# Performance work log

Measured on AMD Instinct MI355X. Metric: run time of the kernel, lower is better.

The kernel has to match this reference:

```python
import jax, jax.numpy as jnp
import numpy as np

N, K = 50000, 64
HID, H = 256, 8
D = HID // H


def setup_inputs() -> dict:
    key = jax.random.key(0)
    ks = jax.random.split(key, 8)
    x = jax.random.normal(ks[0], (N, HID), dtype=jnp.float32)
    neighbor_idx = jax.random.randint(ks[1], (N, K), 0, N, dtype=jnp.int64 if jax.config.jax_enable_x64 else jnp.int32)
    neighbor_mask = jax.random.randint(ks[2], (N, K), 0, 2) == 1  # True = PAD (ignored)
    s = 1.0 / np.sqrt(HID)
    Wq = jax.random.normal(ks[3], (HID, HID), dtype=jnp.float32) * s
    Wk = jax.random.normal(ks[4], (HID, HID), dtype=jnp.float32) * s
    Wv = jax.random.normal(ks[5], (HID, HID), dtype=jnp.float32) * s
    Wo = jax.random.normal(ks[6], (HID, HID), dtype=jnp.float32) * s
    bo = jax.random.normal(ks[7], (HID,), dtype=jnp.float32) * 0.01
    return {"x": x, "neighbor_idx": neighbor_idx, "neighbor_mask": neighbor_mask,
            "Wq": Wq, "Wk": Wk, "Wv": Wv, "Wo": Wo, "bo": bo}


def reference(x, neighbor_idx, neighbor_mask, Wq, Wk, Wv, Wo, bo):
    n, k = neighbor_idx.shape
    scale = jnp.asarray(D, x.dtype) ** -0.5
    # projections (torch nn.Linear: y = x @ W.T)
    q = (x @ Wq.T).reshape(n, H, D)          # [N, H, D]
    k_all = x @ Wk.T                          # [N, HID]
    v_all = x @ Wv.T
    # gather neighbor K/V: [N, k, H, D]
    k_neigh = k_all[neighbor_idx].reshape(n, k, H, D)
    v_neigh = v_all[neighbor_idx].reshape(n, k, H, D)
    # per-node attention scores: [N, H, k]
    scores = jnp.einsum('nhd,nkhd->nhk', q, k_neigh) * scale
    scores = jnp.where(neighbor_mask[:, None, :], -jnp.inf, scores)
    attn = jax.nn.softmax(scores, axis=-1)
    attn = jnp.nan_to_num(attn, nan=0.0)      # rows with all-PAD neighbors -> 0
    out = jnp.einsum('nhk,nkhd->nhd', attn, v_neigh).reshape(n, HID)
    return out @ Wo.T + bo
```

## Files before the change

kernel.cpp:

```cpp
#include <hip/hip_runtime.h>


typedef __bf16 bf16x8 __attribute__((ext_vector_type(8)));
typedef float f32x4 __attribute__((ext_vector_type(4)));
typedef _Float16 h2 __attribute__((ext_vector_type(2)));

#define NN 50000
#define MP 50048
#define MPE ((size_t)MP * 256)
#define QSCALE 0.17677669529663687f

__device__ __forceinline__ float bfl(unsigned u) { return __builtin_bit_cast(float, u << 16); }
__device__ __forceinline__ float bfh(unsigned u) { return __builtin_bit_cast(float, u & 0xFFFF0000u); }
__device__ __forceinline__ unsigned short f2bf(float f) {
    unsigned u = __builtin_bit_cast(unsigned, f);
    return (unsigned short)((u + 0x7FFFu + ((u >> 16) & 1u)) >> 16);
}
__device__ __forceinline__ unsigned pack2(float a, float b) {
    return (unsigned)f2bf(a) | ((unsigned)f2bf(b) << 16);
}
__device__ __forceinline__ void gload16(const void* g, void* l) {
    __builtin_amdgcn_global_load_lds((const __attribute__((address_space(1))) void*)g,
                                     (__attribute__((address_space(3))) void*)l, 16, 0, 0);
}
template <int CTRL>
__device__ __forceinline__ float dpp_add(float x) {
    int yi = __builtin_amdgcn_update_dpp(0, __builtin_bit_cast(int, x), CTRL, 0xF, 0xF, true);
    return x + __builtin_bit_cast(float, yi);
}
template <int CTRL>
__device__ __forceinline__ float dpp_max(float x) {
    int yi = __builtin_amdgcn_update_dpp(0, __builtin_bit_cast(int, x), CTRL, 0xF, 0xF, true);
    return fmaxf(x, __builtin_bit_cast(float, yi));
}
__device__ __forceinline__ float dot2h(unsigned a, unsigned b, float c) {
    return __builtin_amdgcn_fdot2(__builtin_bit_cast(h2, a), __builtin_bit_cast(h2, b), c, false);
}

__global__ __launch_bounds__(256) void prep_k(const float* __restrict__ Wq, const float* __restrict__ Wk,
                                              const float* __restrict__ Wv, const float* __restrict__ Wo,
                                              unsigned short* __restrict__ wqkv, unsigned short* __restrict__ wob,
                                              const void* __restrict__ idxp, const void* __restrict__ maskp,
                                              int* __restrict__ flags) {
    int t = blockIdx.x * 256 + threadIdx.x;
    if (t < 196608) {
        int j = t >> 8, i = t & 255;
        const float* W = (j < 256) ? Wq : (j < 512 ? Wk : Wv);
        wqkv[t] = f2bf(W[((size_t)(j & 255) << 8) | i]);
    } else {
        int u = t - 196608;
        wob[u] = f2bf(Wo[u]);
    }
    if (blockIdx.x == 0) {
        __shared__ int nI32, nF32, nHi;
        if (threadIdx.x == 0) { nI32 = 0; nF32 = 0; nHi = 0; }
        __syncthreads();
        const unsigned* mw = (const unsigned*)maskp;
        const unsigned* iw = (const unsigned*)idxp;
        int a = 0, b = 0, c = 0;
        for (int q = threadIdx.x; q < 1024; q += 256) {
            unsigned v = mw[q];
            if (v > 1u) a = 1;
            if (v != 0u && v != 0x3F800000u) b = 1;
            if (iw[2 * q + 1] != 0u) c = 1;
        }
        if (a) atomicOr(&nI32, 1);
        if (b) atomicOr(&nF32, 1);
        if (c) atomicOr(&nHi, 1);
        __syncthreads();
        if (threadIdx.x == 0) {
            flags[0] = (nI32 == 0) ? 1 : ((nF32 == 0) ? 2 : 0);
            flags[1] = (nHi == 0) ? 1 : 0;
        }
    }
}

__global__ __launch_bounds__(256) void convx_k(const float* __restrict__ x, unsigned short* __restrict__ xb) {
    size_t t = (size_t)blockIdx.x * 256 + threadIdx.x;
    size_t e = t * 8;
    uint4 o;
    if (e < (size_t)NN * 256) {
        float4 a = *(const float4*)&x[e];
        float4 b = *(const float4*)&x[e + 4];
        o.x = pack2(a.x, a.y); o.y = pack2(a.z, a.w);
        o.z = pack2(b.x, b.y); o.w = pack2(b.z, b.w);
    } else {
        o = make_uint4(0, 0, 0, 0);
    }
    *(uint4*)&xb[e] = o;
}

template <int MODE>
__global__ __launch_bounds__(256)
void gemm_bt(const unsigned short* __restrict__ A, const unsigned short* __restrict__ B,
             unsigned short* __restrict__ qkv, float* __restrict__ out, const float* __restrict__ bo) {
    const int tid = threadIdx.x;
    const int wv = tid >> 6, ln = tid & 63;
    const int m0 = blockIdx.x * 128, n0 = blockIdx.y * 128;
    const int wr = wv >> 1, wc = wv & 1;
    __shared__ unsigned short As[2][128][32];
    __shared__ unsigned short Bs[2][128][32];
    f32x4 acc[4][4] = {};

    const int srow = 16 * wv + (ln >> 2);
    #define STAGE(buf, kt)                                                                     \
        {                                                                                      \
            const int col = (kt) * 32 + (ln & 3) * 8;                                          \
            _Pragma("unroll")                                                                  \
            for (int r = 0; r < 2; ++r) {                                                      \
                gload16(&A[(size_t)(m0 + 64 * r + srow) * 256 + col], &As[buf][64 * r + 16 * wv][0]); \
                gload16(&B[(size_t)(n0 + 64 * r + srow) * 256 + col], &Bs[buf][64 * r + 16 * wv][0]); \
            }                                                                                  \
        }

    STAGE(0, 0);
    const int lr = ln & 15, lk = (ln >> 4) * 8;
    for (int kt = 0; kt < 8; ++kt) {
        const int cur = kt & 1;
        __syncthreads();
        if (kt < 7) STAGE(cur ^ 1, kt + 1);
        bf16x8 af[4], bfr[4];
        #pragma unroll
        for (int i = 0; i < 4; ++i) {
            af[i]  = *reinterpret_cast<const bf16x8*>(&As[cur][wr * 64 + i * 16 + lr][lk]);
            bfr[i] = *reinterpret_cast<const bf16x8*>(&Bs[cur][wc * 64 + i * 16 + lr][lk]);
        }
        #pragma unroll
        for (int mi = 0; mi < 4; ++mi)
            #pragma unroll
            for (int ni = 0; ni < 4; ++ni)
                acc[mi][ni] = __builtin_amdgcn_mfma_f32_16x16x32_bf16(af[mi], bfr[ni], acc[mi][ni], 0, 0, 0);
        __syncthreads();
    }

    const int rbase = m0 + wr * 64 + (ln >> 4) * 4;
    const int cbase = n0 + wc * 64 + (ln & 15);
    #pragma unroll
    for (int mi = 0; mi < 4; ++mi) {
        #pragma unroll
        for (int ni = 0; ni < 4; ++ni) {
            const int gn = cbase + ni * 16;
            #pragma unroll
            for (int j = 0; j < 4; ++j) {
                const int gm = rbase + mi * 16 + j;
                float v = acc[mi][ni][j];
                if (MODE == 0) {
                    const float vs = (gn < 256) ? v * QSCALE : v;
                    qkv[(size_t)(gn >> 8) * MPE + (size_t)gm * 256 + (gn & 255)] =
                        __builtin_bit_cast(unsigned short, (_Float16)vs);
                } else {
                    if (gm < NN) out[(size_t)gm * 256 + gn] = v + bo[gn];
                }
            }
        }
    }
    #undef STAGE
}

__global__ __launch_bounds__(256, 3) void attn_k(const unsigned short* __restrict__ qb,
                                                 const unsigned short* __restrict__ kb,
                                                 const unsigned short* __restrict__ vb,
                                                 const void* __restrict__ idxp, const void* __restrict__ maskp,
                                                 unsigned short* __restrict__ attb, const int* __restrict__ flags) {
    const int wv = threadIdx.x >> 6, ln = threadIdx.x & 63;
    const int node = blockIdx.x * 4 + wv;
    const int mlay = flags[0], i64 = flags[1];
    const size_t eb = (size_t)node * 64 + ln;

    int idx = i64 ? ((const int*)idxp)[2 * eb] : ((const int*)idxp)[eb];
    int padi;
    if (mlay == 1)       padi = (((const int*)maskp)[eb] != 0);
    else if (mlay == 2)  padi = (((const unsigned*)maskp)[eb] != 0u);
    else                 padi = (((const unsigned char*)maskp)[eb] != 0);
    const unsigned long long pm = __ballot(padi);
    const int idx_eff = padi ? node : idx;

    const uint2 qv = *(const uint2*)&qb[(size_t)node * 256 + ln * 4];

    const int p = ln & 7;

    uint2 ka[64];
    #pragma unroll
    for (int k = 0; k < 64; ++k) {
        const unsigned nk = (unsigned)__builtin_amdgcn_readlane(idx_eff, k);
        ka[k] = *((const uint2*)(kb + ((size_t)nk << 8)) + ln);
    }
    __builtin_amdgcn_sched_barrier(0);

    float s[8];
    #pragma unroll
    for (int k = 0; k < 64; ++k) {
        const uint2 kv = ka[k];
        float part = dot2h(qv.x, kv.x, dot2h(qv.y, kv.y, 0.0f));
        part = dpp_add<0xB1>(part);
        part = dpp_add<0x4E>(part);
        part = dpp_add<0x141>(part);
        const float sc = ((pm >> k) & 1ull) ? -1e30f : part;
        if ((k & 7) == p) s[k >> 3] = sc;
    }

    uint2 va[64];
    #pragma unroll
    for (int k = 0; k < 64; ++k) {
        const unsigned nk = (unsigned)__builtin_amdgcn_readlane(idx_eff, k);
        va[k] = *((const uint2*)(vb + ((size_t)nk << 8)) + ln);
    }
    __builtin_amdgcn_sched_barrier(0);

    float m = s[0];
    #pragma unroll
    for (int r = 1; r < 8; ++r) m = fmaxf(m, s[r]);
    m = dpp_max<0xB1>(m); m = dpp_max<0x4E>(m); m = dpp_max<0x141>(m);
    float w[8], sum = 0.f;
    #pragma unroll
    for (int r = 0; r < 8; ++r) { w[r] = __expf(s[r] - m); sum += w[r]; }
    sum = dpp_add<0xB1>(sum); sum = dpp_add<0x4E>(sum); sum = dpp_add<0x141>(sum);
    const float inv = (m > -1e29f && sum > 0.f) ? 1.0f / sum : 0.0f;
    #pragma unroll
    for (int r = 0; r < 8; ++r) w[r] *= inv;

    float o0 = 0.f, o1 = 0.f, o2 = 0.f, o3 = 0.f;
    const int baddr = (ln & 56) * 4;
    #pragma unroll
    for (int k = 0; k < 64; ++k) {
        const int wi = __builtin_amdgcn_ds_bpermute(baddr + 4 * (k & 7),
                                                    __builtin_bit_cast(int, w[k >> 3]));
        const float wk = __builtin_bit_cast(float, wi);
        const h2 vx = __builtin_bit_cast(h2, va[k].x);
        const h2 vy = __builtin_bit_cast(h2, va[k].y);
        o0 += wk * (float)vx.x; o1 += wk * (float)vx.y;
        o2 += wk * (float)vy.x; o3 += wk * (float)vy.y;
    }
    uint2 ov;
    ov.x = pack2(o0, o1);
    ov.y = pack2(o2, o3);
    *(uint2*)&attb[(size_t)node * 256 + ln * 4] = ov;
}

extern "C" void kernel_launch(void* const* d_in, const int* in_sizes, int n_in,
                              void* d_out, int out_size, void* d_ws, size_t ws_size,
                              hipStream_t stream) {
    const float* x   = (const float*)d_in[0];
    const void*  idx = d_in[1];
    const void*  msk = d_in[2];
    const float* Wq  = (const float*)d_in[3];
    const float* Wk  = (const float*)d_in[4];
    const float* Wv  = (const float*)d_in[5];
    const float* Wo  = (const float*)d_in[6];
    const float* bo  = (const float*)d_in[7];
    float* out = (float*)d_out;

    unsigned short* xb   = (unsigned short*)d_ws;
    unsigned short* qb   = xb + MPE;
    unsigned short* kb   = qb + MPE;
    unsigned short* vb   = kb + MPE;
    unsigned short* attb = vb + MPE;
    unsigned short* wqkv = attb + MPE;
    unsigned short* wob  = wqkv + 768 * 256;
    int* flags = (int*)(wob + 256 * 256);

    prep_k<<<1024, 256, 0, stream>>>(Wq, Wk, Wv, Wo, wqkv, wob, idx, msk, flags);
    convx_k<<<6256, 256, 0, stream>>>(x, xb);
    gemm_bt<0><<<dim3(391, 6), 256, 0, stream>>>(xb, wqkv, qb, nullptr, nullptr);
    attn_k<<<12500, 256, 0, stream>>>(qb, kb, vb, idx, msk, attb, flags);
    gemm_bt<1><<<dim3(391, 2), 256, 0, stream>>>(attb, wob, nullptr, out, bo);
}
```

Baseline: 430.8 us.

## Restructure QK scoring so each lane computes full per-head dots with pipelined K loads

```diff
diff --git a/kernel.cpp b/kernel.cpp
--- a/kernel.cpp
+++ b/kernel.cpp
@@ -173,31 +173,55 @@
     else if (mlay == 2)  padi = (((const unsigned*)maskp)[eb] != 0u);
     else                 padi = (((const unsigned char*)maskp)[eb] != 0);
     const unsigned long long pm = __ballot(padi);
-    const int idx_eff = padi ? node : idx;
-
-    const uint2 qv = *(const uint2*)&qb[(size_t)node * 256 + ln * 4];
-
-    const int p = ln & 7;
-
-    uint2 ka[64];
-    #pragma unroll
-    for (int k = 0; k < 64; ++k) {
-        const unsigned nk = (unsigned)__builtin_amdgcn_readlane(idx_eff, k);
-        ka[k] = *((const uint2*)(kb + ((size_t)nk << 8)) + ln);
-    }
+    int idx_eff = padi ? node : idx;
+
+    const int h = ln >> 3, j = ln & 7;
+    const int hoff = h << 6;
+    const unsigned mlo = (unsigned)pm, mhi = (unsigned)(pm >> 32);
+
+    const char* qrow = (const char*)qb + (((size_t)node) << 9) + hoff;
+    const uint4 q0 = *(const uint4*)(qrow);
+    const uint4 q1 = *(const uint4*)(qrow + 16);
+    const uint4 q2 = *(const uint4*)(qrow + 32);
+    const uint4 q3 = *(const uint4*)(qrow + 48);
+
+    const char* kbase = (const char*)kb;
+    uint4 kr[3][4];
+    #define KISSUE(buf, c)                                                                \
+        {                                                                                 \
+            const int nk = __builtin_amdgcn_ds_bpermute(4 * j + 32 * (c), idx_eff);       \
+            const unsigned vo = ((unsigned)nk << 9) + hoff;                               \
+            kr[buf][0] = *(const uint4*)(kbase + vo);                                     \
+            kr[buf][1] = *(const uint4*)(kbase + vo + 16);                                \
+            kr[buf][2] = *(const uint4*)(kbase + vo + 32);                                \
+            kr[buf][3] = *(const uint4*)(kbase + vo + 48);                                \
+        }
+    KISSUE(0, 0)
+    KISSUE(1, 1)
     __builtin_amdgcn_sched_barrier(0);
 
     float s[8];
     #pragma unroll
-    for (int k = 0; k < 64; ++k) {
-        const uint2 kv = ka[k];
-        float part = dot2h(qv.x, kv.x, dot2h(qv.y, kv.y, 0.0f));
-        part = dpp_add<0xB1>(part);
-        part = dpp_add<0x4E>(part);
-        part = dpp_add<0x141>(part);
-        const float sc = ((pm >> k) & 1ull) ? -1e30f : part;
-        if ((k & 7) == p) s[k >> 3] = sc;
-    }
+    for (int c = 0; c < 8; ++c) {
+        if (c < 6) { KISSUE((c + 2) % 3, c + 2) }
+        __builtin_amdgcn_sched_barrier(0);
+        const int cb = c % 3;
+        float a0 = dot2h(q0.x, kr[cb][0].x, 0.f);
+        float a1 = dot2h(q1.x, kr[cb][1].x, 0.f);
+        float a2 = dot2h(q2.x, kr[cb][2].x, 0.f);
+        float a3 = dot2h(q3.x, kr[cb][3].x, 0.f);
+        a0 = dot2h(q0.y, kr[cb][0].y, a0); a1 = dot2h(q1.y, kr[cb][1].y, a1);
+        a2 = dot2h(q2.y, kr[cb][2].y, a2); a3 = dot2h(q3.y, kr[cb][3].y, a3);
+        a0 = dot2h(q0.z, kr[cb][0].z, a0); a1 = dot2h(q1.z, kr[cb][1].z, a1);
+        a2 = dot2h(q2.z, kr[cb][2].z, a2); a3 = dot2h(q3.z, kr[cb][3].z, a3);
+        a0 = dot2h(q0.w, kr[cb][0].w, a0); a1 = dot2h(q1.w, kr[cb][1].w, a1);
+        a2 = dot2h(q2.w, kr[cb][2].w, a2); a3 = dot2h(q3.w, kr[cb][3].w, a3);
+        const float dot = (a0 + a1) + (a2 + a3);
+        const unsigned word = (c < 4) ? mlo : mhi;
+        const unsigned bit = (word >> (((8 * c) & 31) + j)) & 1u;
+        s[c] = bit ? -1e30f : dot;
+    }
+    #undef KISSUE
 
     uint2 va[64];
     #pragma unroll
@@ -216,8 +240,6 @@
     for (int r = 0; r < 8; ++r) { w[r] = __expf(s[r] - m); sum += w[r]; }
     sum = dpp_add<0xB1>(sum); sum = dpp_add<0x4E>(sum); sum = dpp_add<0x141>(sum);
     const float inv = (m > -1e29f && sum > 0.f) ? 1.0f / sum : 0.0f;
-    #pragma unroll
-    for (int r = 0; r < 8; ++r) w[r] *= inv;
 
     float o0 = 0.f, o1 = 0.f, o2 = 0.f, o3 = 0.f;
     const int baddr = (ln & 56) * 4;
@@ -232,8 +254,8 @@
         o2 += wk * (float)vy.x; o3 += wk * (float)vy.y;
     }
     uint2 ov;
-    ov.x = pack2(o0, o1);
-    ov.y = pack2(o2, o3);
+    ov.x = pack2(o0 * inv, o1 * inv);
+    ov.y = pack2(o2 * inv, o3 * inv);
     *(uint2*)&attb[(size_t)node * 256 + ln * 4] = ov;
 }
 
```

Measured after the change: 436.9 us. Within noise of the previous version (+1.4%).

## Widen GEMM K-tile to 64 with XOR-swizzled LDS and XCD-aware block remap

Applied to the files above, without the earlier changes.

```diff
diff --git a/kernel.cpp b/kernel.cpp
--- a/kernel.cpp
+++ b/kernel.cpp
@@ -90,46 +90,60 @@
     *(uint4*)&xb[e] = o;
 }
 
-template <int MODE>
+template <int MODE, int NY, int NWG>
 __global__ __launch_bounds__(256)
 void gemm_bt(const unsigned short* __restrict__ A, const unsigned short* __restrict__ B,
              unsigned short* __restrict__ qkv, float* __restrict__ out, const float* __restrict__ bo) {
+    constexpr int Q = NWG / 8, R = NWG % 8;
+    const int f = blockIdx.x;
+    const int xcd = f & 7, pos = f >> 3;
+    const int wgid = (xcd < R ? xcd * (Q + 1) : R * (Q + 1) + (xcd - R) * Q) + pos;
+    const int m0 = (wgid / NY) * 128, n0 = (wgid % NY) * 128;
+
     const int tid = threadIdx.x;
     const int wv = tid >> 6, ln = tid & 63;
-    const int m0 = blockIdx.x * 128, n0 = blockIdx.y * 128;
     const int wr = wv >> 1, wc = wv & 1;
-    __shared__ unsigned short As[2][128][32];
-    __shared__ unsigned short Bs[2][128][32];
+    __shared__ unsigned short As[2][128][64];
+    __shared__ unsigned short Bs[2][128][64];
     f32x4 acc[4][4] = {};
 
-    const int srow = 16 * wv + (ln >> 2);
-    #define STAGE(buf, kt)                                                                     \
-        {                                                                                      \
-            const int col = (kt) * 32 + (ln & 3) * 8;                                          \
-            _Pragma("unroll")                                                                  \
-            for (int r = 0; r < 2; ++r) {                                                      \
-                gload16(&A[(size_t)(m0 + 64 * r + srow) * 256 + col], &As[buf][64 * r + 16 * wv][0]); \
-                gload16(&B[(size_t)(n0 + 64 * r + srow) * 256 + col], &Bs[buf][64 * r + 16 * wv][0]); \
-            }                                                                                  \
+    const int srow = 8 * wv + (ln >> 3);
+    const int scolE = (((ln & 7) ^ (ln >> 3)) << 3);
+    #define STAGE(buf, kt)                                                                      \
+        {                                                                                       \
+            _Pragma("unroll")                                                                   \
+            for (int r = 0; r < 4; ++r) {                                                       \
+                gload16(&A[(size_t)(m0 + 32 * r + srow) * 256 + (kt) * 64 + scolE],             \
+                        &As[buf][32 * r + 8 * wv][0]);                                          \
+                gload16(&B[(size_t)(n0 + 32 * r + srow) * 256 + (kt) * 64 + scolE],             \
+                        &Bs[buf][32 * r + 8 * wv][0]);                                          \
+            }                                                                                   \
         }
 
     STAGE(0, 0);
-    const int lr = ln & 15, lk = (ln >> 4) * 8;
-    for (int kt = 0; kt < 8; ++kt) {
+    const int lr = ln & 15;
+    const int lkb = (ln >> 4) * 16;
+    const int swz = (ln & 7) << 4;
+    for (int kt = 0; kt < 4; ++kt) {
         const int cur = kt & 1;
         __syncthreads();
-        if (kt < 7) STAGE(cur ^ 1, kt + 1);
-        bf16x8 af[4], bfr[4];
+        if (kt < 3) STAGE(cur ^ 1, kt + 1);
         #pragma unroll
-        for (int i = 0; i < 4; ++i) {
-            af[i]  = *reinterpret_cast<const bf16x8*>(&As[cur][wr * 64 + i * 16 + lr][lk]);
-            bfr[i] = *reinterpret_cast<const bf16x8*>(&Bs[cur][wc * 64 + i * 16 + lr][lk]);
-        }
-        #pragma unroll
-        for (int mi = 0; mi < 4; ++mi)
+        for (int k2 = 0; k2 < 2; ++k2) {
+            bf16x8 af[4], bfr[4];
             #pragma unroll
-            for (int ni = 0; ni < 4; ++ni)
-                acc[mi][ni] = __builtin_amdgcn_mfma_f32_16x16x32_bf16(af[mi], bfr[ni], acc[mi][ni], 0, 0, 0);
+            for (int i = 0; i < 4; ++i) {
+                af[i]  = *reinterpret_cast<const bf16x8*>(
+                    (const char*)&As[cur][wr * 64 + i * 16 + lr][0] + ((k2 * 64 + lkb) ^ swz));
+                bfr[i] = *reinterpret_cast<const bf16x8*>(
+                    (const char*)&Bs[cur][wc * 64 + i * 16 + lr][0] + ((k2 * 64 + lkb) ^ swz));
+            }
+            #pragma unroll
+            for (int mi = 0; mi < 4; ++mi)
+                #pragma unroll
+                for (int ni = 0; ni < 4; ++ni)
+                    acc[mi][ni] = __builtin_amdgcn_mfma_f32_16x16x32_bf16(af[mi], bfr[ni], acc[mi][ni], 0, 0, 0);
+        }
         __syncthreads();
     }
 
@@ -261,7 +275,7 @@
 
     prep_k<<<1024, 256, 0, stream>>>(Wq, Wk, Wv, Wo, wqkv, wob, idx, msk, flags);
     convx_k<<<6256, 256, 0, stream>>>(x, xb);
-    gemm_bt<0><<<dim3(391, 6), 256, 0, stream>>>(xb, wqkv, qb, nullptr, nullptr);
+    gemm_bt<0, 6, 2346><<<2346, 256, 0, stream>>>(xb, wqkv, qb, nullptr, nullptr);
     attn_k<<<12500, 256, 0, stream>>>(qb, kb, vb, idx, msk, attb, flags);
-    gemm_bt<1><<<dim3(391, 2), 256, 0, stream>>>(attb, wob, nullptr, out, bo);
-}
+    gemm_bt<1, 2, 782><<<782, 256, 0, stream>>>(attb, wob, nullptr, out, bo);
+}
```

Measured after the change: 417.6 us. -3.1%, faster.
